# Optimization experiments

Measured on AMD Instinct MI355X. Metric: run time of the kernel, lower is better.

Reference implementation:

```python
import jax, jax.numpy as jnp
import numpy as np

TAU = 2.0      # LIF membrane time constant
ALPHA = 4.0    # spikingjelly surrogate.Sigmoid default alpha
EPS = 1e-5     # BatchNorm eps
HEADS = 8

@jax.custom_vjp
def heaviside(x):
    return (x >= 0).astype(x.dtype)

def _hv_fwd(x):
    return (x >= 0).astype(x.dtype), x

def _hv_bwd(x, g):
    s = jax.nn.sigmoid(ALPHA * x)
    return (g * ALPHA * s * (1.0 - s),)

heaviside.defvjp(_hv_fwd, _hv_bwd)

def lif(x, vth=1.0):
    # multi-step LIF, decay_input=True, v_reset=0 (hard reset), detach_reset=True
    def step(v, xt):
        v = v + (xt - v) / TAU
        s = heaviside(v - vth)
        v = v * (1.0 - jax.lax.stop_gradient(s))
        return v, s
    _, spikes = jax.lax.scan(step, jnp.zeros_like(x[0]), x)
    return spikes

def bn(x, gamma, beta, mean, var):
    # x: [T,B,C,N]; eval-mode BatchNorm1d over channel axis 2
    inv = gamma * jax.lax.rsqrt(var + EPS)
    return x * inv[None, None, :, None] + (beta - mean * inv)[None, None, :, None]

def conv1x1(x, w):
    # x: [T,B,C,N], w: [Cout,Cin] (Conv1d kernel_size=1)
    return jnp.einsum('tbcn,dc->tbdn', x, w)

def setup_inputs():
    key = jax.random.key(0)
    ks = jax.random.split(key, 24)
    T, B, C, H, W = 4, 16, 512, 32, 32
    scale = 1.0 / np.sqrt(C)
    d = {}
    d['x'] = jax.random.normal(ks[0], (T, B, C, H, W), jnp.float32)
    def bn_params(i):
        g = 1.0 + 0.1 * jax.random.normal(ks[i], (C,), jnp.float32)
        b = 0.1 * jax.random.normal(ks[i + 1], (C,), jnp.float32)
        m = 0.1 * jax.random.normal(ks[i + 2], (C,), jnp.float32)
        v = jax.random.uniform(ks[i + 3], (C,), jnp.float32, 0.5, 1.5)
        return g, b, m, v
    d['q_w'] = scale * jax.random.normal(ks[1], (C, C), jnp.float32)
    d['q_gamma'], d['q_beta'], d['q_mean'], d['q_var'] = bn_params(2)
    d['k_w'] = scale * jax.random.normal(ks[6], (C, C), jnp.float32)
    d['k_gamma'], d['k_beta'], d['k_mean'], d['k_var'] = bn_params(7)
    d['proj_w'] = scale * jax.random.normal(ks[11], (C, C), jnp.float32)
    d['proj_b'] = 0.01 * jax.random.normal(ks[12], (C,), jnp.float32)
    d['p_gamma'], d['p_beta'], d['p_mean'], d['p_var'] = bn_params(13)
    return d

def reference(x, q_w, q_gamma, q_beta, q_mean, q_var,
              k_w, k_gamma, k_beta, k_mean, k_var,
              proj_w, proj_b, p_gamma, p_beta, p_mean, p_var):
    T, B, C, H, W = x.shape
    N = H * W
    Dh = C // HEADS
    xs = lif(x).reshape(T, B, C, N)                    # shortcut_lif then flatten(3)
    q = lif(bn(conv1x1(xs, q_w), q_gamma, q_beta, q_mean, q_var))
    k = lif(bn(conv1x1(xs, k_w), k_gamma, k_beta, k_mean, k_var))
    qh = q.reshape(T, B, HEADS, Dh, N).sum(axis=3, keepdims=True)  # [T,B,h,1,N]
    attn = lif(qh, vth=0.5)
    kh = k.reshape(T, B, HEADS, Dh, N)
    y = (attn * kh).reshape(T, B, C, N)
    y = bn(conv1x1(y, proj_w) + proj_b[None, None, :, None],
           p_gamma, p_beta, p_mean, p_var)
    return y.reshape(T, B, C, H, W), attn
```

## Files before the change

kernel.cpp:

```cpp
#include <hip/hip_runtime.h>

typedef unsigned short u16;
typedef unsigned int u32;
typedef float f32x4 __attribute__((ext_vector_type(4)));
typedef short s16x8 __attribute__((ext_vector_type(8)));

#define T_ 4
#define B_ 16
#define C_ 512
#define N_ 1024
#define YSZ 33554432

__device__ __forceinline__ u16 f2bf(float f) {
  u32 u = __float_as_uint(f);
  u32 r = u + 0x7FFFu + ((u >> 16) & 1u);
  return (u16)(r >> 16);
}
__device__ __forceinline__ float bf2f(u16 h) { return __uint_as_float(((u32)h) << 16); }

__device__ __forceinline__ void async16(const void* g, void* l) {
  __builtin_amdgcn_global_load_lds((const __attribute__((address_space(1))) void*)g,
                                   (__attribute__((address_space(3))) void*)l, 16, 0, 0);
}

__global__ void prep_kernel(const float* __restrict__ qw, const float* __restrict__ kw,
                            const float* __restrict__ pw,
                            const float* __restrict__ qg, const float* __restrict__ qb,
                            const float* __restrict__ qm, const float* __restrict__ qv,
                            const float* __restrict__ kg, const float* __restrict__ kb,
                            const float* __restrict__ km, const float* __restrict__ kv,
                            const float* __restrict__ pg, const float* __restrict__ pbt,
                            const float* __restrict__ pm, const float* __restrict__ pv,
                            u16* __restrict__ whlq, u16* __restrict__ whlk,
                            u16* __restrict__ pwb, float* __restrict__ consts) {
  int blk = blockIdx.x, tid = threadIdx.x;
  if (blk < 512) {
    int d = blk;
    for (int c = tid; c < 512; c += 256) {
      float w = qw[d * 512 + c];
      u16 hi = f2bf(w);
      whlq[d * 1024 + c] = hi;
      whlq[d * 1024 + 512 + c] = f2bf(w - bf2f(hi));
      w = kw[d * 512 + c];
      hi = f2bf(w);
      whlk[d * 1024 + c] = hi;
      whlk[d * 1024 + 512 + c] = f2bf(w - bf2f(hi));
      pwb[d * 512 + c] = f2bf(pw[d * 512 + c]);
    }
  } else {
    for (int c = tid; c < 512; c += 256) {
      float inv = qg[c] / sqrtf(qv[c] + 1e-5f);
      consts[c] = inv; consts[512 + c] = qb[c] - qm[c] * inv;
      inv = kg[c] / sqrtf(kv[c] + 1e-5f);
      consts[1024 + c] = inv; consts[1536 + c] = kb[c] - km[c] * inv;
      inv = pg[c] / sqrtf(pv[c] + 1e-5f);
      consts[2048 + c] = inv; consts[2560 + c] = pbt[c] - pm[c] * inv;
    }
  }
}

__global__ __launch_bounds__(256) void lifx_kernel(const float* __restrict__ x,
                                                   u16* __restrict__ xs) {
  int b = blockIdx.z;
  int cbase = blockIdx.y * 64, nbase = blockIdx.x * 64;
  int tid = threadIdx.x;
  int c_l = tid >> 6, n_l = tid & 63;
  __shared__ __align__(16) u16 tile[64 * 72];
  float v[16];
#pragma unroll
  for (int i = 0; i < 16; ++i) v[i] = 0.f;
  for (int t = 0; t < 4; ++t) {
    const float* xp = x + ((size_t)(t * 16 + b) * 512 + cbase + c_l * 16) * 1024 + nbase + n_l;
#pragma unroll
    for (int i = 0; i < 16; ++i) {
      float xv = xp[(size_t)i * 1024];
      float vn = v[i] + 0.5f * (xv - v[i]);
      bool s = vn >= 1.0f;
      tile[n_l * 72 + c_l * 16 + i] = s ? 0x3F80 : 0;
      v[i] = s ? 0.f : vn;
    }
    __syncthreads();
    u16* yb = xs + ((size_t)(t * 16 + b) * 1024 + nbase) * 512 + cbase;
#pragma unroll
    for (int e = 0; e < 2; ++e) {
      int chunk = tid * 2 + e;
      int n = chunk >> 3, c0 = (chunk & 7) * 8;
      *(uint4*)&yb[(size_t)n * 512 + c0] = *(const uint4*)&tile[n * 72 + c0];
    }
    __syncthreads();
  }
}

__global__ __launch_bounds__(256, 2) void gemm_q_kernel(
    const u16* __restrict__ A, const u16* __restrict__ Bbase,
    const float* __restrict__ consts, float* __restrict__ dout) {
  const int tid = threadIdx.x;
  const int lane = tid & 63, w = tid >> 6;
  const int wm = w >> 1, wn = w & 1;
  const int quad = lane >> 4, l16 = lane & 15;
  const int b = blockIdx.z;
  const int m_blk = blockIdx.y * 128, n_blk = blockIdx.x * 128;
  const int srow = lane >> 3;
  const int scol = (((lane & 7) ^ srow) & 7) * 8;
  __shared__ __align__(16) u16 smem[3 * 128 * 64];
  u16* Ash = smem;
  u16* Asl = smem + 8192;
  u16* Bs  = smem + 16384;
  const int rxor = l16 & 7;
  float v[64];
#pragma unroll
  for (int i = 0; i < 64; ++i) v[i] = 0.f;
  float va[4] = {0.f, 0.f, 0.f, 0.f};

  for (int t = 0; t < 4; ++t) {
    f32x4 acc[4][4];
    const f32x4 zero = {0.f, 0.f, 0.f, 0.f};
#pragma unroll
    for (int i = 0; i < 4; ++i)
#pragma unroll
      for (int j = 0; j < 4; ++j) acc[i][j] = zero;
    const u16* Bt = Bbase + (size_t)(t * 16 + b) * (N_ * C_);

    for (int k0 = 0; k0 < 512; k0 += 64) {
#pragma unroll
      for (int i = 0; i < 4; ++i) {
        int r = i * 32 + w * 8 + srow;
        int lo = (i * 32 + w * 8) * 64;
        async16(A + (size_t)(m_blk + r) * 1024 + k0 + scol, &Ash[lo]);
        async16(A + (size_t)(m_blk + r) * 1024 + 512 + k0 + scol, &Asl[lo]);
        async16(Bt + (size_t)(n_blk + r) * 512 + k0 + scol, &Bs[lo]);
      }
      __syncthreads();
#pragma unroll
      for (int kk = 0; kk < 2; ++kk) {
        s16x8 ah[4], al[4], bf[4];
        const int slot = ((kk * 4 + quad) ^ rxor) * 8;
#pragma unroll
        for (int ti = 0; ti < 4; ++ti) {
          ah[ti] = *(const s16x8*)&Ash[(wm * 64 + ti * 16 + l16) * 64 + slot];
          al[ti] = *(const s16x8*)&Asl[(wm * 64 + ti * 16 + l16) * 64 + slot];
        }
#pragma unroll
        for (int tj = 0; tj < 4; ++tj)
          bf[tj] = *(const s16x8*)&Bs[(wn * 64 + tj * 16 + l16) * 64 + slot];
#pragma unroll
        for (int ti = 0; ti < 4; ++ti)
#pragma unroll
          for (int tj = 0; tj < 4; ++tj) {
            acc[ti][tj] = __builtin_amdgcn_mfma_f32_16x16x32_bf16(ah[ti], bf[tj], acc[ti][tj], 0, 0, 0);
            acc[ti][tj] = __builtin_amdgcn_mfma_f32_16x16x32_bf16(al[ti], bf[tj], acc[ti][tj], 0, 0, 0);
          }
      }
      __syncthreads();
    }

    float qp[4] = {0.f, 0.f, 0.f, 0.f};
#pragma unroll
    for (int ti = 0; ti < 4; ++ti) {
#pragma unroll
      for (int r = 0; r < 4; ++r) {
        int row = m_blk + wm * 64 + ti * 16 + quad * 4 + r;
        float iv = consts[row], ib = consts[512 + row];
#pragma unroll
        for (int tj = 0; tj < 4; ++tj) {
          float bnv = acc[ti][tj][r] * iv + ib;
          float vv = v[(ti * 4 + tj) * 4 + r];
          float vn = vv + 0.5f * (bnv - vv);
          bool s = vn >= 1.0f;
          v[(ti * 4 + tj) * 4 + r] = s ? 0.f : vn;
          qp[tj] += s ? 1.f : 0.f;
        }
      }
    }
    int h = (m_blk >> 6) + wm;
#pragma unroll
    for (int tj = 0; tj < 4; ++tj) {
      float q = qp[tj];
      q += __shfl_xor(q, 16, 64);
      q += __shfl_xor(q, 32, 64);
      float vn = va[tj] + 0.5f * (q - va[tj]);
      bool s = vn >= 0.5f;
      va[tj] = s ? 0.f : vn;
      if (quad == 0) {
        int col = n_blk + wn * 64 + tj * 16 + l16;
        dout[(size_t)YSZ + ((size_t)(t * 16 + b) * 8 + h) * 1024 + col] = s ? 1.f : 0.f;
      }
    }
  }
}

__global__ __launch_bounds__(256, 2) void gemm_k_kernel(
    const u16* __restrict__ A, const u16* __restrict__ Bbase,
    const float* __restrict__ consts, const float* __restrict__ dout,
    u16* __restrict__ y) {
  const int tid = threadIdx.x;
  const int lane = tid & 63, w = tid >> 6;
  const int wm = w >> 1, wn = w & 1;
  const int quad = lane >> 4, l16 = lane & 15;
  const int b = blockIdx.z;
  const int m_blk = blockIdx.y * 128, n_blk = blockIdx.x * 128;
  const int srow = lane >> 3;
  const int scol = (((lane & 7) ^ srow) & 7) * 8;
  __shared__ __align__(16) u16 smem[3 * 128 * 64];
  u16* Ash = smem;
  u16* Asl = smem + 8192;
  u16* Bs  = smem + 16384;
  u16* Ys  = smem;
  const int rxor = l16 & 7;
  float v[64];
#pragma unroll
  for (int i = 0; i < 64; ++i) v[i] = 0.f;

  for (int t = 0; t < 4; ++t) {
    f32x4 acc[4][4];
    const f32x4 zero = {0.f, 0.f, 0.f, 0.f};
#pragma unroll
    for (int i = 0; i < 4; ++i)
#pragma unroll
      for (int j = 0; j < 4; ++j) acc[i][j] = zero;
    const u16* Bt = Bbase + (size_t)(t * 16 + b) * (N_ * C_);

    for (int k0 = 0; k0 < 512; k0 += 64) {
#pragma unroll
      for (int i = 0; i < 4; ++i) {
        int r = i * 32 + w * 8 + srow;
        int lo = (i * 32 + w * 8) * 64;
        async16(A + (size_t)(m_blk + r) * 1024 + k0 + scol, &Ash[lo]);
        async16(A + (size_t)(m_blk + r) * 1024 + 512 + k0 + scol, &Asl[lo]);
        async16(Bt + (size_t)(n_blk + r) * 512 + k0 + scol, &Bs[lo]);
      }
      __syncthreads();
#pragma unroll
      for (int kk = 0; kk < 2; ++kk) {
        s16x8 ah[4], al[4], bf[4];
        const int slot = ((kk * 4 + quad) ^ rxor) * 8;
#pragma unroll
        for (int ti = 0; ti < 4; ++ti) {
          ah[ti] = *(const s16x8*)&Ash[(wm * 64 + ti * 16 + l16) * 64 + slot];
          al[ti] = *(const s16x8*)&Asl[(wm * 64 + ti * 16 + l16) * 64 + slot];
        }
#pragma unroll
        for (int tj = 0; tj < 4; ++tj)
          bf[tj] = *(const s16x8*)&Bs[(wn * 64 + tj * 16 + l16) * 64 + slot];
#pragma unroll
        for (int ti = 0; ti < 4; ++ti)
#pragma unroll
          for (int tj = 0; tj < 4; ++tj) {
            acc[ti][tj] = __builtin_amdgcn_mfma_f32_16x16x32_bf16(ah[ti], bf[tj], acc[ti][tj], 0, 0, 0);
            acc[ti][tj] = __builtin_amdgcn_mfma_f32_16x16x32_bf16(al[ti], bf[tj], acc[ti][tj], 0, 0, 0);
          }
      }
      __syncthreads();
    }

    int h = (m_blk >> 6) + wm;
    float at[4];
#pragma unroll
    for (int tj = 0; tj < 4; ++tj) {
      int col = n_blk + wn * 64 + tj * 16 + l16;
      at[tj] = dout[(size_t)YSZ + ((size_t)(t * 16 + b) * 8 + h) * 1024 + col];
    }

#pragma unroll
    for (int ti = 0; ti < 4; ++ti) {
      u16 pk[4][4];
#pragma unroll
      for (int r = 0; r < 4; ++r) {
        int row = m_blk + wm * 64 + ti * 16 + quad * 4 + r;
        float iv = consts[1024 + row], ib = consts[1536 + row];
#pragma unroll
        for (int tj = 0; tj < 4; ++tj) {
          float bnv = acc[ti][tj][r] * iv + ib;
          float vv = v[(ti * 4 + tj) * 4 + r];
          float vn = vv + 0.5f * (bnv - vv);
          bool s = vn >= 1.0f;
          v[(ti * 4 + tj) * 4 + r] = s ? 0.f : vn;
          pk[tj][r] = (s && at[tj] != 0.f) ? 0x3F80 : 0;
        }
      }
#pragma unroll
      for (int tj = 0; tj < 4; ++tj) {
        int n_loc = wn * 64 + tj * 16 + l16;
        int c_loc = wm * 64 + ti * 16 + quad * 4;
        u32 lo2 = (u32)pk[tj][0] | ((u32)pk[tj][1] << 16);
        u32 hi2 = (u32)pk[tj][2] | ((u32)pk[tj][3] << 16);
        uint2 pv2; pv2.x = lo2; pv2.y = hi2;
        *(uint2*)&Ys[n_loc * 132 + c_loc] = pv2;
      }
    }
    __syncthreads();
    u16* yb = y + ((size_t)(t * 16 + b) * 1024 + n_blk) * 512 + m_blk;
#pragma unroll
    for (int p = 0; p < 8; ++p) {
      int idx = p * 256 + tid;
      int rown = idx >> 4, ch = (idx & 15) * 8;
      *(uint4*)&yb[(size_t)rown * 512 + ch] = *(const uint4*)&Ys[rown * 132 + ch];
    }
    __syncthreads();
  }
}

__global__ __launch_bounds__(256, 3) void gemm_proj_kernel(
    const u16* __restrict__ A, const u16* __restrict__ Bbase,
    float* __restrict__ outP, const float* __restrict__ projb,
    const float* __restrict__ consts) {
  const int tid = threadIdx.x;
  const int lane = tid & 63, w = tid >> 6;
  const int wm = w >> 1, wn = w & 1;
  const int quad = lane >> 4, l16 = lane & 15;
  const int tb = blockIdx.z;
  const int m_blk = blockIdx.y * 128, n_blk = blockIdx.x * 128;
  const int srow = lane >> 3;
  const int scol = (((lane & 7) ^ srow) & 7) * 8;
  __shared__ __align__(16) u16 As[128 * 64];
  __shared__ __align__(16) u16 Bs[128 * 64];
  f32x4 acc[4][4];
  const f32x4 zero = {0.f, 0.f, 0.f, 0.f};
#pragma unroll
  for (int i = 0; i < 4; ++i)
#pragma unroll
    for (int j = 0; j < 4; ++j) acc[i][j] = zero;
  const u16* Bt = Bbase + (size_t)tb * (N_ * C_);
  const int rxor = l16 & 7;

  for (int k0 = 0; k0 < 512; k0 += 64) {
#pragma unroll
    for (int i = 0; i < 4; ++i) {
      int r = i * 32 + w * 8 + srow;
      async16(A + (size_t)(m_blk + r) * 512 + k0 + scol, &As[(i * 32 + w * 8) * 64]);
      async16(Bt + (size_t)(n_blk + r) * 512 + k0 + scol, &Bs[(i * 32 + w * 8) * 64]);
    }
    __syncthreads();
#pragma unroll
    for (int kk = 0; kk < 2; ++kk) {
      s16x8 af[4], bf[4];
      const int slot = ((kk * 4 + quad) ^ rxor) * 8;
#pragma unroll
      for (int ti = 0; ti < 4; ++ti)
        af[ti] = *(const s16x8*)&As[(wm * 64 + ti * 16 + l16) * 64 + slot];
#pragma unroll
      for (int tj = 0; tj < 4; ++tj)
        bf[tj] = *(const s16x8*)&Bs[(wn * 64 + tj * 16 + l16) * 64 + slot];
#pragma unroll
      for (int ti = 0; ti < 4; ++ti)
#pragma unroll
        for (int tj = 0; tj < 4; ++tj)
          acc[ti][tj] = __builtin_amdgcn_mfma_f32_16x16x32_bf16(af[ti], bf[tj], acc[ti][tj], 0, 0, 0);
    }
    __syncthreads();
  }

  const float* pinv = consts + 2048;
  const float* pb2 = consts + 2560;
  float* o = outP + (size_t)tb * (C_ * N_);
#pragma unroll
  for (int ti = 0; ti < 4; ++ti) {
    int row0 = m_blk + wm * 64 + ti * 16 + quad * 4;
#pragma unroll
    for (int r = 0; r < 4; ++r) {
      int row = row0 + r;
      float bi = projb[row], piv = pinv[row], pbi = pb2[row];
#pragma unroll
      for (int tj = 0; tj < 4; ++tj) {
        int col = n_blk + wn * 64 + tj * 16 + l16;
        o[(size_t)row * N_ + col] = (acc[ti][tj][r] + bi) * piv + pbi;
      }
    }
  }
}

extern "C" void kernel_launch(void* const* d_in, const int* in_sizes, int n_in,
                              void* d_out, int out_size, void* d_ws, size_t ws_size,
                              hipStream_t stream) {
  const float* x   = (const float*)d_in[0];
  const float* qw  = (const float*)d_in[1];
  const float* qg  = (const float*)d_in[2];
  const float* qb  = (const float*)d_in[3];
  const float* qm  = (const float*)d_in[4];
  const float* qv  = (const float*)d_in[5];
  const float* kw  = (const float*)d_in[6];
  const float* kg  = (const float*)d_in[7];
  const float* kb  = (const float*)d_in[8];
  const float* km  = (const float*)d_in[9];
  const float* kv  = (const float*)d_in[10];
  const float* pw  = (const float*)d_in[11];
  const float* pb  = (const float*)d_in[12];
  const float* pg  = (const float*)d_in[13];
  const float* pbt = (const float*)d_in[14];
  const float* pm  = (const float*)d_in[15];
  const float* pv  = (const float*)d_in[16];
  float* out = (float*)d_out;
  char* ws = (char*)d_ws;

  u16* xs       = (u16*)ws;
  u16* y2       = (u16*)(ws + 67108864);
  u16* whlq     = (u16*)(ws + 201326592);
  u16* whlk     = (u16*)(ws + 202375168);
  u16* pwb      = (u16*)(ws + 203423744);
  float* consts = (float*)(ws + 203948032);

  prep_kernel<<<513, 256, 0, stream>>>(qw, kw, pw, qg, qb, qm, qv, kg, kb, km, kv,
                                       pg, pbt, pm, pv, whlq, whlk, pwb, consts);
  lifx_kernel<<<dim3(16, 8, 16), 256, 0, stream>>>(x, xs);
  gemm_q_kernel<<<dim3(8, 4, 16), 256, 0, stream>>>(whlq, xs, consts, out);
  gemm_k_kernel<<<dim3(8, 4, 16), 256, 0, stream>>>(whlk, xs, consts, out, y2);
  gemm_proj_kernel<<<dim3(8, 4, 64), 256, 0, stream>>>(pwb, y2, out, pb, consts);
}
```

Before: 428.7 us.

## Double-buffer Q/K GEMM mainloop with larger 128x256 tiles and 8 waves

```diff
diff --git a/kernel.cpp b/kernel.cpp
--- a/kernel.cpp
+++ b/kernel.cpp
@@ -22,6 +22,25 @@
   __builtin_amdgcn_global_load_lds((const __attribute__((address_space(1))) void*)g,
                                    (__attribute__((address_space(3))) void*)l, 16, 0, 0);
 }
+
+#define LDV(p) (*(const s16x8*)(p))
+#define MFMA_(a, b, c) __builtin_amdgcn_mfma_f32_16x16x32_bf16(a, b, c, 0, 0, 0)
+
+#define MFMA16(P)                                                                      \
+  do {                                                                                 \
+    acc[P][0] = MFMA_(ahA, bf0, acc[P][0]); acc[P][0] = MFMA_(alA, bf0, acc[P][0]);    \
+    acc[P][1] = MFMA_(ahA, bf1, acc[P][1]); acc[P][1] = MFMA_(alA, bf1, acc[P][1]);    \
+    acc[P][2] = MFMA_(ahA, bf2, acc[P][2]); acc[P][2] = MFMA_(alA, bf2, acc[P][2]);    \
+    acc[P][3] = MFMA_(ahA, bf3, acc[P][3]); acc[P][3] = MFMA_(alA, bf3, acc[P][3]);    \
+    acc[(P)+1][0] = MFMA_(ahB, bf0, acc[(P)+1][0]);                                    \
+    acc[(P)+1][0] = MFMA_(alB, bf0, acc[(P)+1][0]);                                    \
+    acc[(P)+1][1] = MFMA_(ahB, bf1, acc[(P)+1][1]);                                    \
+    acc[(P)+1][1] = MFMA_(alB, bf1, acc[(P)+1][1]);                                    \
+    acc[(P)+1][2] = MFMA_(ahB, bf2, acc[(P)+1][2]);                                    \
+    acc[(P)+1][2] = MFMA_(alB, bf2, acc[(P)+1][2]);                                    \
+    acc[(P)+1][3] = MFMA_(ahB, bf3, acc[(P)+1][3]);                                    \
+    acc[(P)+1][3] = MFMA_(alB, bf3, acc[(P)+1][3]);                                    \
+  } while (0)
 
 __global__ void prep_kernel(const float* __restrict__ qw, const float* __restrict__ kw,
                             const float* __restrict__ pw,
@@ -91,21 +110,113 @@
   }
 }
 
-__global__ __launch_bounds__(256, 2) void gemm_q_kernel(
+__device__ __forceinline__ void qk_mainloop(
+    const u16* __restrict__ A, const u16* __restrict__ Bt, u16* sm,
+    int m_blk, int n_blk, int wid, int wm, int wn, int quad, int l16,
+    int srow, int scol, int rxor, f32x4 (&acc)[4][4]) {
+  const int aoff = (wm * 64 + l16) * 64;
+  const int boff = 16384 + (wn * 64 + l16) * 64;
+  const int slot0 = (quad ^ rxor) * 8;
+  const int slot1 = ((4 + quad) ^ rxor) * 8;
+  const int arow = wid * 8 + srow;
+
+#pragma unroll
+  for (int j = 0; j < 2; ++j) {
+    const u16* src = A + (size_t)(m_blk + j * 64 + arow) * 1024 + scol;
+    async16(src,       sm + (j * 8 + wid) * 512);
+    async16(src + 512, sm + 8192 + (j * 8 + wid) * 512);
+  }
+#pragma unroll
+  for (int j = 0; j < 4; ++j)
+    async16(Bt + (size_t)(n_blk + j * 64 + arow) * 512 + scol,
+            sm + 16384 + (j * 8 + wid) * 512);
+  __syncthreads();
+
+  int cur = 0;
+  for (int s = 0; s < 8; ++s) {
+    u16* S = sm + cur * 32768;
+    u16* Sn = sm + (cur ^ 1) * 32768;
+    const int k0n = (s + 1) * 64;
+    const bool pf = (s < 7);
+    s16x8 ahA, ahB, alA, alB, bf0, bf1, bf2, bf3;
+
+    ahA = LDV(S + aoff + slot0);
+    ahB = LDV(S + aoff + 1024 + slot0);
+    alA = LDV(S + 8192 + aoff + slot0);
+    alB = LDV(S + 8192 + aoff + 1024 + slot0);
+    bf0 = LDV(S + boff + slot0);
+    bf1 = LDV(S + boff + 1024 + slot0);
+    bf2 = LDV(S + boff + 2048 + slot0);
+    bf3 = LDV(S + boff + 3072 + slot0);
+    if (pf) {
+#pragma unroll
+      for (int j = 0; j < 2; ++j) {
+        const u16* src = A + (size_t)(m_blk + j * 64 + arow) * 1024 + k0n + scol;
+        async16(src,       Sn + (j * 8 + wid) * 512);
+        async16(src + 512, Sn + 8192 + (j * 8 + wid) * 512);
+      }
+    }
+    __builtin_amdgcn_s_barrier();
+    __builtin_amdgcn_s_setprio(1);
+    MFMA16(0);
+    __builtin_amdgcn_s_setprio(0);
+    __builtin_amdgcn_s_barrier();
+
+    ahA = LDV(S + aoff + 2048 + slot0);
+    ahB = LDV(S + aoff + 3072 + slot0);
+    alA = LDV(S + 8192 + aoff + 2048 + slot0);
+    alB = LDV(S + 8192 + aoff + 3072 + slot0);
+    if (pf) {
+#pragma unroll
+      for (int j = 0; j < 4; ++j)
+        async16(Bt + (size_t)(n_blk + j * 64 + arow) * 512 + k0n + scol,
+                Sn + 16384 + (j * 8 + wid) * 512);
+    }
+    __builtin_amdgcn_s_barrier();
+    __builtin_amdgcn_s_setprio(1);
+    MFMA16(2);
+    __builtin_amdgcn_s_setprio(0);
+    __builtin_amdgcn_s_barrier();
+
+    ahA = LDV(S + aoff + slot1);
+    ahB = LDV(S + aoff + 1024 + slot1);
+    alA = LDV(S + 8192 + aoff + slot1);
+    alB = LDV(S + 8192 + aoff + 1024 + slot1);
+    bf0 = LDV(S + boff + slot1);
+    bf1 = LDV(S + boff + 1024 + slot1);
+    bf2 = LDV(S + boff + 2048 + slot1);
+    bf3 = LDV(S + boff + 3072 + slot1);
+    __builtin_amdgcn_s_barrier();
+    __builtin_amdgcn_s_setprio(1);
+    MFMA16(0);
+    __builtin_amdgcn_s_setprio(0);
+    __builtin_amdgcn_s_barrier();
+
+    ahA = LDV(S + aoff + 2048 + slot1);
+    ahB = LDV(S + aoff + 3072 + slot1);
+    alA = LDV(S + 8192 + aoff + 2048 + slot1);
+    alB = LDV(S + 8192 + aoff + 3072 + slot1);
+    __builtin_amdgcn_s_barrier();
+    __builtin_amdgcn_s_setprio(1);
+    MFMA16(2);
+    __builtin_amdgcn_s_setprio(0);
+    __syncthreads();
+    cur ^= 1;
+  }
+}
+
+__global__ __launch_bounds__(512, 2) void gemm_q_kernel(
     const u16* __restrict__ A, const u16* __restrict__ Bbase,
     const float* __restrict__ consts, float* __restrict__ dout) {
+  extern __shared__ u16 sm[];
   const int tid = threadIdx.x;
-  const int lane = tid & 63, w = tid >> 6;
-  const int wm = w >> 1, wn = w & 1;
+  const int lane = tid & 63, wid = tid >> 6;
+  const int wm = wid >> 2, wn = wid & 3;
   const int quad = lane >> 4, l16 = lane & 15;
   const int b = blockIdx.z;
-  const int m_blk = blockIdx.y * 128, n_blk = blockIdx.x * 128;
+  const int m_blk = blockIdx.y * 128, n_blk = blockIdx.x * 256;
   const int srow = lane >> 3;
   const int scol = (((lane & 7) ^ srow) & 7) * 8;
-  __shared__ __align__(16) u16 smem[3 * 128 * 64];
-  u16* Ash = smem;
-  u16* Asl = smem + 8192;
-  u16* Bs  = smem + 16384;
   const int rxor = l16 & 7;
   float v[64];
 #pragma unroll
@@ -121,38 +232,7 @@
       for (int j = 0; j < 4; ++j) acc[i][j] = zero;
     const u16* Bt = Bbase + (size_t)(t * 16 + b) * (N_ * C_);
 
-    for (int k0 = 0; k0 < 512; k0 += 64) {
-#pragma unroll
-      for (int i = 0; i < 4; ++i) {
-        int r = i * 32 + w * 8 + srow;
-        int lo = (i * 32 + w * 8) * 64;
-        async16(A + (size_t)(m_blk + r) * 1024 + k0 + scol, &Ash[lo]);
-        async16(A + (size_t)(m_blk + r) * 1024 + 512 + k0 + scol, &Asl[lo]);
-        async16(Bt + (size_t)(n_blk + r) * 512 + k0 + scol, &Bs[lo]);
-      }
-      __syncthreads();
-#pragma unroll
-      for (int kk = 0; kk < 2; ++kk) {
-        s16x8 ah[4], al[4], bf[4];
-        const int slot = ((kk * 4 + quad) ^ rxor) * 8;
-#pragma unroll
-        for (int ti = 0; ti < 4; ++ti) {
-          ah[ti] = *(const s16x8*)&Ash[(wm * 64 + ti * 16 + l16) * 64 + slot];
-          al[ti] = *(const s16x8*)&Asl[(wm * 64 + ti * 16 + l16) * 64 + slot];
-        }
-#pragma unroll
-        for (int tj = 0; tj < 4; ++tj)
-          bf[tj] = *(const s16x8*)&Bs[(wn * 64 + tj * 16 + l16) * 64 + slot];
-#pragma unroll
-        for (int ti = 0; ti < 4; ++ti)
-#pragma unroll
-          for (int tj = 0; tj < 4; ++tj) {
-            acc[ti][tj] = __builtin_amdgcn_mfma_f32_16x16x32_bf16(ah[ti], bf[tj], acc[ti][tj], 0, 0, 0);
-            acc[ti][tj] = __builtin_amdgcn_mfma_f32_16x16x32_bf16(al[ti], bf[tj], acc[ti][tj], 0, 0, 0);
-          }
-      }
-      __syncthreads();
-    }
+    qk_mainloop(A, Bt, sm, m_blk, n_blk, wid, wm, wn, quad, l16, srow, scol, rxor, acc);
 
     float qp[4] = {0.f, 0.f, 0.f, 0.f};
 #pragma unroll
@@ -189,23 +269,19 @@
   }
 }
 
-__global__ __launch_bounds__(256, 2) void gemm_k_kernel(
+__global__ __launch_bounds__(512, 2) void gemm_k_kernel(
     const u16* __restrict__ A, const u16* __restrict__ Bbase,
     const float* __restrict__ consts, const float* __restrict__ dout,
     u16* __restrict__ y) {
+  extern __shared__ u16 sm[];
   const int tid = threadIdx.x;
-  const int lane = tid & 63, w = tid >> 6;
-  const int wm = w >> 1, wn = w & 1;
+  const int lane = tid & 63, wid = tid >> 6;
+  const int wm = wid >> 2, wn = wid & 3;
   const int quad = lane >> 4, l16 = lane & 15;
   const int b = blockIdx.z;
-  const int m_blk = blockIdx.y * 128, n_blk = blockIdx.x * 128;
+  const int m_blk = blockIdx.y * 128, n_blk = blockIdx.x * 256;
   const int srow = lane >> 3;
   const int scol = (((lane & 7) ^ srow) & 7) * 8;
-  __shared__ __align__(16) u16 smem[3 * 128 * 64];
-  u16* Ash = smem;
-  u16* Asl = smem + 8192;
-  u16* Bs  = smem + 16384;
-  u16* Ys  = smem;
   const int rxor = l16 & 7;
   float v[64];
 #pragma unroll
@@ -220,38 +296,7 @@
       for (int j = 0; j < 4; ++j) acc[i][j] = zero;
     const u16* Bt = Bbase + (size_t)(t * 16 + b) * (N_ * C_);
 
-    for (int k0 = 0; k0 < 512; k0 += 64) {
-#pragma unroll
-      for (int i = 0; i < 4; ++i) {
-        int r = i * 32 + w * 8 + srow;
-        int lo = (i * 32 + w * 8) * 64;
-        async16(A + (size_t)(m_blk + r) * 1024 + k0 + scol, &Ash[lo]);
-        async16(A + (size_t)(m_blk + r) * 1024 + 512 + k0 + scol, &Asl[lo]);
-        async16(Bt + (size_t)(n_blk + r) * 512 + k0 + scol, &Bs[lo]);
-      }
-      __syncthreads();
-#pragma unroll
-      for (int kk = 0; kk < 2; ++kk) {
-        s16x8 ah[4], al[4], bf[4];
-        const int slot = ((kk * 4 + quad) ^ rxor) * 8;
-#pragma unroll
-        for (int ti = 0; ti < 4; ++ti) {
-          ah[ti] = *(const s16x8*)&Ash[(wm * 64 + ti * 16 + l16) * 64 + slot];
-          al[ti] = *(const s16x8*)&Asl[(wm * 64 + ti * 16 + l16) * 64 + slot];
-        }
-#pragma unroll
-        for (int tj = 0; tj < 4; ++tj)
-          bf[tj] = *(const s16x8*)&Bs[(wn * 64 + tj * 16 + l16) * 64 + slot];
-#pragma unroll
-        for (int ti = 0; ti < 4; ++ti)
-#pragma unroll
-          for (int tj = 0; tj < 4; ++tj) {
-            acc[ti][tj] = __builtin_amdgcn_mfma_f32_16x16x32_bf16(ah[ti], bf[tj], acc[ti][tj], 0, 0, 0);
-            acc[ti][tj] = __builtin_amdgcn_mfma_f32_16x16x32_bf16(al[ti], bf[tj], acc[ti][tj], 0, 0, 0);
-          }
-      }
-      __syncthreads();
-    }
+    qk_mainloop(A, Bt, sm, m_blk, n_blk, wid, wm, wn, quad, l16, srow, scol, rxor, acc);
 
     int h = (m_blk >> 6) + wm;
     float at[4];
@@ -261,6 +306,7 @@
       at[tj] = dout[(size_t)YSZ + ((size_t)(t * 16 + b) * 8 + h) * 1024 + col];
     }
 
+    u16* Ys = sm;
 #pragma unroll
     for (int ti = 0; ti < 4; ++ti) {
       u16 pk[4][4];
@@ -292,7 +338,7 @@
     u16* yb = y + ((size_t)(t * 16 + b) * 1024 + n_blk) * 512 + m_blk;
 #pragma unroll
     for (int p = 0; p < 8; ++p) {
-      int idx = p * 256 + tid;
+      int idx = p * 512 + tid;
       int rown = idx >> 4, ch = (idx & 15) * 8;
       *(uint4*)&yb[(size_t)rown * 512 + ch] = *(const uint4*)&Ys[rown * 132 + ch];
     }
@@ -399,10 +445,19 @@
   u16* pwb      = (u16*)(ws + 203423744);
   float* consts = (float*)(ws + 203948032);
 
+  static int attr_done = 0;
+  if (!attr_done) {
+    hipFuncSetAttribute((const void*)gemm_q_kernel,
+                        hipFuncAttributeMaxDynamicSharedMemorySize, 131072);
+    hipFuncSetAttribute((const void*)gemm_k_kernel,
+                        hipFuncAttributeMaxDynamicSharedMemorySize, 131072);
+    attr_done = 1;
+  }
+
   prep_kernel<<<513, 256, 0, stream>>>(qw, kw, pw, qg, qb, qm, qv, kg, kb, km, kv,
                                        pg, pbt, pm, pv, whlq, whlk, pwb, consts);
   lifx_kernel<<<dim3(16, 8, 16), 256, 0, stream>>>(x, xs);
-  gemm_q_kernel<<<dim3(8, 4, 16), 256, 0, stream>>>(whlq, xs, consts, out);
-  gemm_k_kernel<<<dim3(8, 4, 16), 256, 0, stream>>>(whlk, xs, consts, out, y2);
+  gemm_q_kernel<<<dim3(4, 4, 16), 512, 131072, stream>>>(whlq, xs, consts, out);
+  gemm_k_kernel<<<dim3(4, 4, 16), 512, 131072, stream>>>(whlk, xs, consts, out, y2);
   gemm_proj_kernel<<<dim3(8, 4, 64), 256, 0, stream>>>(pwb, y2, out, pb, consts);
 }
```

Measured after the change: 508.2 us. +18.5%, slower.

## Store binary spike tensors as packed bitmasks and expand in registers

Applied to the files above, without the earlier changes.

```diff
diff --git a/kernel.cpp b/kernel.cpp
--- a/kernel.cpp
+++ b/kernel.cpp
@@ -1,5 +1,6 @@
 #include <hip/hip_runtime.h>
 
+typedef unsigned char u8;
 typedef unsigned short u16;
 typedef unsigned int u32;
 typedef float f32x4 __attribute__((ext_vector_type(4)));
@@ -21,6 +22,15 @@
 __device__ __forceinline__ void async16(const void* g, void* l) {
   __builtin_amdgcn_global_load_lds((const __attribute__((address_space(1))) void*)g,
                                    (__attribute__((address_space(3))) void*)l, 16, 0, 0);
+}
+
+__device__ __forceinline__ s16x8 expand8(u32 m) {
+  union { u32 w[4]; s16x8 v; } u;
+  u.w[0] = (m & 1u   ? 0x3F80u : 0u) | (m & 2u   ? 0x3F800000u : 0u);
+  u.w[1] = (m & 4u   ? 0x3F80u : 0u) | (m & 8u   ? 0x3F800000u : 0u);
+  u.w[2] = (m & 16u  ? 0x3F80u : 0u) | (m & 32u  ? 0x3F800000u : 0u);
+  u.w[3] = (m & 64u  ? 0x3F80u : 0u) | (m & 128u ? 0x3F800000u : 0u);
+  return u.v;
 }
 
 __global__ void prep_kernel(const float* __restrict__ qw, const float* __restrict__ kw,
@@ -60,39 +70,32 @@
 }
 
 __global__ __launch_bounds__(256) void lifx_kernel(const float* __restrict__ x,
-                                                   u16* __restrict__ xs) {
+                                                   u8* __restrict__ xsb) {
   int b = blockIdx.z;
   int cbase = blockIdx.y * 64, nbase = blockIdx.x * 64;
   int tid = threadIdx.x;
   int c_l = tid >> 6, n_l = tid & 63;
-  __shared__ __align__(16) u16 tile[64 * 72];
   float v[16];
 #pragma unroll
   for (int i = 0; i < 16; ++i) v[i] = 0.f;
   for (int t = 0; t < 4; ++t) {
     const float* xp = x + ((size_t)(t * 16 + b) * 512 + cbase + c_l * 16) * 1024 + nbase + n_l;
+    u32 mask = 0;
 #pragma unroll
     for (int i = 0; i < 16; ++i) {
       float xv = xp[(size_t)i * 1024];
       float vn = v[i] + 0.5f * (xv - v[i]);
       bool s = vn >= 1.0f;
-      tile[n_l * 72 + c_l * 16 + i] = s ? 0x3F80 : 0;
+      mask |= (s ? 1u : 0u) << i;
       v[i] = s ? 0.f : vn;
     }
-    __syncthreads();
-    u16* yb = xs + ((size_t)(t * 16 + b) * 1024 + nbase) * 512 + cbase;
-#pragma unroll
-    for (int e = 0; e < 2; ++e) {
-      int chunk = tid * 2 + e;
-      int n = chunk >> 3, c0 = (chunk & 7) * 8;
-      *(uint4*)&yb[(size_t)n * 512 + c0] = *(const uint4*)&tile[n * 72 + c0];
-    }
-    __syncthreads();
+    *(u16*)&xsb[((size_t)(t * 16 + b) * 1024 + nbase + n_l) * 64 + (cbase >> 3) + c_l * 2] =
+        (u16)mask;
   }
 }
 
 __global__ __launch_bounds__(256, 2) void gemm_q_kernel(
-    const u16* __restrict__ A, const u16* __restrict__ Bbase,
+    const u16* __restrict__ A, const u8* __restrict__ xsb,
     const float* __restrict__ consts, float* __restrict__ dout) {
   const int tid = threadIdx.x;
   const int lane = tid & 63, w = tid >> 6;
@@ -102,11 +105,11 @@
   const int m_blk = blockIdx.y * 128, n_blk = blockIdx.x * 128;
   const int srow = lane >> 3;
   const int scol = (((lane & 7) ^ srow) & 7) * 8;
-  __shared__ __align__(16) u16 smem[3 * 128 * 64];
+  __shared__ __align__(16) u16 smem[2 * 8192];
   u16* Ash = smem;
   u16* Asl = smem + 8192;
-  u16* Bs  = smem + 16384;
   const int rxor = l16 & 7;
+  const int brow = n_blk + wn * 64 + l16;
   float v[64];
 #pragma unroll
   for (int i = 0; i < 64; ++i) v[i] = 0.f;
@@ -119,7 +122,7 @@
     for (int i = 0; i < 4; ++i)
 #pragma unroll
       for (int j = 0; j < 4; ++j) acc[i][j] = zero;
-    const u16* Bt = Bbase + (size_t)(t * 16 + b) * (N_ * C_);
+    const u8* bitsT = xsb + (size_t)(t * 16 + b) * (N_ * 64);
 
     for (int k0 = 0; k0 < 512; k0 += 64) {
 #pragma unroll
@@ -128,8 +131,11 @@
         int lo = (i * 32 + w * 8) * 64;
         async16(A + (size_t)(m_blk + r) * 1024 + k0 + scol, &Ash[lo]);
         async16(A + (size_t)(m_blk + r) * 1024 + 512 + k0 + scol, &Asl[lo]);
-        async16(Bt + (size_t)(n_blk + r) * 512 + k0 + scol, &Bs[lo]);
-      }
+      }
+      uint2 g[4];
+#pragma unroll
+      for (int tj = 0; tj < 4; ++tj)
+        g[tj] = *(const uint2*)&bitsT[(size_t)(brow + tj * 16) * 64 + (k0 >> 3)];
       __syncthreads();
 #pragma unroll
       for (int kk = 0; kk < 2; ++kk) {
@@ -141,8 +147,10 @@
           al[ti] = *(const s16x8*)&Asl[(wm * 64 + ti * 16 + l16) * 64 + slot];
         }
 #pragma unroll
-        for (int tj = 0; tj < 4; ++tj)
-          bf[tj] = *(const s16x8*)&Bs[(wn * 64 + tj * 16 + l16) * 64 + slot];
+        for (int tj = 0; tj < 4; ++tj) {
+          u32 wb = kk ? g[tj].y : g[tj].x;
+          bf[tj] = expand8((wb >> (quad * 8)) & 0xFFu);
+        }
 #pragma unroll
         for (int ti = 0; ti < 4; ++ti)
 #pragma unroll
@@ -190,9 +198,9 @@
 }
 
 __global__ __launch_bounds__(256, 2) void gemm_k_kernel(
-    const u16* __restrict__ A, const u16* __restrict__ Bbase,
+    const u16* __restrict__ A, const u8* __restrict__ xsb,
     const float* __restrict__ consts, const float* __restrict__ dout,
-    u16* __restrict__ y) {
+    u8* __restrict__ y2b) {
   const int tid = threadIdx.x;
   const int lane = tid & 63, w = tid >> 6;
   const int wm = w >> 1, wn = w & 1;
@@ -201,12 +209,12 @@
   const int m_blk = blockIdx.y * 128, n_blk = blockIdx.x * 128;
   const int srow = lane >> 3;
   const int scol = (((lane & 7) ^ srow) & 7) * 8;
-  __shared__ __align__(16) u16 smem[3 * 128 * 64];
+  __shared__ __align__(16) u16 smem[2 * 8192];
   u16* Ash = smem;
   u16* Asl = smem + 8192;
-  u16* Bs  = smem + 16384;
-  u16* Ys  = smem;
+  u16* Ysb = smem;
   const int rxor = l16 & 7;
+  const int brow = n_blk + wn * 64 + l16;
   float v[64];
 #pragma unroll
   for (int i = 0; i < 64; ++i) v[i] = 0.f;
@@ -218,7 +226,7 @@
     for (int i = 0; i < 4; ++i)
 #pragma unroll
       for (int j = 0; j < 4; ++j) acc[i][j] = zero;
-    const u16* Bt = Bbase + (size_t)(t * 16 + b) * (N_ * C_);
+    const u8* bitsT = xsb + (size_t)(t * 16 + b) * (N_ * 64);
 
     for (int k0 = 0; k0 < 512; k0 += 64) {
 #pragma unroll
@@ -227,8 +235,11 @@
         int lo = (i * 32 + w * 8) * 64;
         async16(A + (size_t)(m_blk + r) * 1024 + k0 + scol, &Ash[lo]);
         async16(A + (size_t)(m_blk + r) * 1024 + 512 + k0 + scol, &Asl[lo]);
-        async16(Bt + (size_t)(n_blk + r) * 512 + k0 + scol, &Bs[lo]);
-      }
+      }
+      uint2 g[4];
+#pragma unroll
+      for (int tj = 0; tj < 4; ++tj)
+        g[tj] = *(const uint2*)&bitsT[(size_t)(brow + tj * 16) * 64 + (k0 >> 3)];
       __syncthreads();
 #pragma unroll
       for (int kk = 0; kk < 2; ++kk) {
@@ -240,8 +251,10 @@
           al[ti] = *(const s16x8*)&Asl[(wm * 64 + ti * 16 + l16) * 64 + slot];
         }
 #pragma unroll
-        for (int tj = 0; tj < 4; ++tj)
-          bf[tj] = *(const s16x8*)&Bs[(wn * 64 + tj * 16 + l16) * 64 + slot];
+        for (int tj = 0; tj < 4; ++tj) {
+          u32 wb = kk ? g[tj].y : g[tj].x;
+          bf[tj] = expand8((wb >> (quad * 8)) & 0xFFu);
+        }
 #pragma unroll
         for (int ti = 0; ti < 4; ++ti)
 #pragma unroll
@@ -263,7 +276,7 @@
 
 #pragma unroll
     for (int ti = 0; ti < 4; ++ti) {
-      u16 pk[4][4];
+      u32 nib[4] = {0u, 0u, 0u, 0u};
 #pragma unroll
       for (int r = 0; r < 4; ++r) {
         int row = m_blk + wm * 64 + ti * 16 + quad * 4 + r;
@@ -275,33 +288,35 @@
           float vn = vv + 0.5f * (bnv - vv);
           bool s = vn >= 1.0f;
           v[(ti * 4 + tj) * 4 + r] = s ? 0.f : vn;
-          pk[tj][r] = (s && at[tj] != 0.f) ? 0x3F80 : 0;
+          nib[tj] |= (s && at[tj] != 0.f) ? (1u << r) : 0u;
         }
       }
 #pragma unroll
       for (int tj = 0; tj < 4; ++tj) {
-        int n_loc = wn * 64 + tj * 16 + l16;
-        int c_loc = wm * 64 + ti * 16 + quad * 4;
-        u32 lo2 = (u32)pk[tj][0] | ((u32)pk[tj][1] << 16);
-        u32 hi2 = (u32)pk[tj][2] | ((u32)pk[tj][3] << 16);
-        uint2 pv2; pv2.x = lo2; pv2.y = hi2;
-        *(uint2*)&Ys[n_loc * 132 + c_loc] = pv2;
+        u32 v16 = nib[tj] | (((u32)__shfl_xor((int)nib[tj], 16, 64)) << 4);
+        v16 = v16 | (((u32)__shfl_xor((int)v16, 32, 64)) << 8);
+        if (quad == 0) {
+          int n_loc = wn * 64 + tj * 16 + l16;
+          Ysb[n_loc * 10 + wm * 4 + ti] = (u16)v16;
+        }
       }
     }
     __syncthreads();
-    u16* yb = y + ((size_t)(t * 16 + b) * 1024 + n_blk) * 512 + m_blk;
-#pragma unroll
-    for (int p = 0; p < 8; ++p) {
-      int idx = p * 256 + tid;
-      int rown = idx >> 4, ch = (idx & 15) * 8;
-      *(uint4*)&yb[(size_t)rown * 512 + ch] = *(const uint4*)&Ys[rown * 132 + ch];
+    {
+      u8* yb = y2b + ((size_t)(t * 16 + b) * 1024 + n_blk) * 64 + (m_blk >> 3);
+      int rown = tid >> 1, half = tid & 1;
+      const u16* src = &Ysb[rown * 10 + half * 4];
+      uint2 pv;
+      pv.x = (u32)src[0] | ((u32)src[1] << 16);
+      pv.y = (u32)src[2] | ((u32)src[3] << 16);
+      *(uint2*)&yb[(size_t)rown * 64 + half * 8] = pv;
     }
     __syncthreads();
   }
 }
 
 __global__ __launch_bounds__(256, 3) void gemm_proj_kernel(
-    const u16* __restrict__ A, const u16* __restrict__ Bbase,
+    const u16* __restrict__ A, const u8* __restrict__ y2b,
     float* __restrict__ outP, const float* __restrict__ projb,
     const float* __restrict__ consts) {
   const int tid = threadIdx.x;
@@ -313,23 +328,26 @@
   const int srow = lane >> 3;
   const int scol = (((lane & 7) ^ srow) & 7) * 8;
   __shared__ __align__(16) u16 As[128 * 64];
-  __shared__ __align__(16) u16 Bs[128 * 64];
   f32x4 acc[4][4];
   const f32x4 zero = {0.f, 0.f, 0.f, 0.f};
 #pragma unroll
   for (int i = 0; i < 4; ++i)
 #pragma unroll
     for (int j = 0; j < 4; ++j) acc[i][j] = zero;
-  const u16* Bt = Bbase + (size_t)tb * (N_ * C_);
+  const u8* bitsT = y2b + (size_t)tb * (N_ * 64);
   const int rxor = l16 & 7;
+  const int browb = n_blk + wn * 64 + l16;
 
   for (int k0 = 0; k0 < 512; k0 += 64) {
 #pragma unroll
     for (int i = 0; i < 4; ++i) {
       int r = i * 32 + w * 8 + srow;
       async16(A + (size_t)(m_blk + r) * 512 + k0 + scol, &As[(i * 32 + w * 8) * 64]);
-      async16(Bt + (size_t)(n_blk + r) * 512 + k0 + scol, &Bs[(i * 32 + w * 8) * 64]);
-    }
+    }
+    uint2 g[4];
+#pragma unroll
+    for (int tj = 0; tj < 4; ++tj)
+      g[tj] = *(const uint2*)&bitsT[(size_t)(browb + tj * 16) * 64 + (k0 >> 3)];
     __syncthreads();
 #pragma unroll
     for (int kk = 0; kk < 2; ++kk) {
@@ -339,8 +357,10 @@
       for (int ti = 0; ti < 4; ++ti)
         af[ti] = *(const s16x8*)&As[(wm * 64 + ti * 16 + l16) * 64 + slot];
 #pragma unroll
-      for (int tj = 0; tj < 4; ++tj)
-        bf[tj] = *(const s16x8*)&Bs[(wn * 64 + tj * 16 + l16) * 64 + slot];
+      for (int tj = 0; tj < 4; ++tj) {
+        u32 wbits = kk ? g[tj].y : g[tj].x;
+        bf[tj] = expand8((wbits >> (quad * 8)) & 0xFFu);
+      }
 #pragma unroll
       for (int ti = 0; ti < 4; ++ti)
 #pragma unroll
@@ -392,17 +412,17 @@
   float* out = (float*)d_out;
   char* ws = (char*)d_ws;
 
-  u16* xs       = (u16*)ws;
-  u16* y2       = (u16*)(ws + 67108864);
-  u16* whlq     = (u16*)(ws + 201326592);
-  u16* whlk     = (u16*)(ws + 202375168);
-  u16* pwb      = (u16*)(ws + 203423744);
-  float* consts = (float*)(ws + 203948032);
+  u8*  xsb      = (u8*)ws;
+  u8*  y2b      = (u8*)(ws + 4194304);
+  u16* whlq     = (u16*)(ws + 8388608);
+  u16* whlk     = (u16*)(ws + 9437184);
+  u16* pwb      = (u16*)(ws + 10485760);
+  float* consts = (float*)(ws + 11010048);
 
   prep_kernel<<<513, 256, 0, stream>>>(qw, kw, pw, qg, qb, qm, qv, kg, kb, km, kv,
                                        pg, pbt, pm, pv, whlq, whlk, pwb, consts);
-  lifx_kernel<<<dim3(16, 8, 16), 256, 0, stream>>>(x, xs);
-  gemm_q_kernel<<<dim3(8, 4, 16), 256, 0, stream>>>(whlq, xs, consts, out);
-  gemm_k_kernel<<<dim3(8, 4, 16), 256, 0, stream>>>(whlk, xs, consts, out, y2);
-  gemm_proj_kernel<<<dim3(8, 4, 64), 256, 0, stream>>>(pwb, y2, out, pb, consts);
-}
+  lifx_kernel<<<dim3(16, 8, 16), 256, 0, stream>>>(x, xsb);
+  gemm_q_kernel<<<dim3(8, 4, 16), 256, 0, stream>>>(whlq, xsb, consts, out);
+  gemm_k_kernel<<<dim3(8, 4, 16), 256, 0, stream>>>(whlk, xsb, consts, out, y2b);
+  gemm_proj_kernel<<<dim3(8, 4, 64), 256, 0, stream>>>(pwb, y2b, out, pb, consts);
+}
```

New measurement: 449.6 us. 4.9% more time.
